# Optimization experiments

Measured on AMD Instinct MI355X. Metric: run time of the kernel, lower is better.

The kernel has to match this reference:

```python
import jax, jax.numpy as jnp
import numpy as np
from jax import lax

INT8_NARROW = (-127.0, 127.0)   # brevitas Int8WeightPerTensorFloat (narrow range)
INT8_FULL = (-128.0, 127.0)     # brevitas Int8ActPerTensorFloat
INT32 = (-2.0**31, 2.0**31 - 1)


def _fake_quant(v, scale, qmin, qmax):
    # round-to-nearest, clip, dequant (per-tensor)
    return jnp.clip(jnp.round(v / scale), qmin, qmax) * scale


def _conv(x, w, stride):
    return lax.conv_general_dilated(
        x, w, window_strides=(stride, stride), padding=[(1, 1), (1, 1)],
        dimension_numbers=("NCHW", "OIHW", "NCHW"))


def setup_inputs() -> dict:
    key = jax.random.key(0)
    ks = jax.random.split(key, 5)
    B, Cin, Cout, H = 64, 256, 512, 28
    x = jax.random.normal(ks[0], (B, Cin, H, H), dtype=jnp.float32)
    w1 = jax.random.normal(ks[1], (Cout, Cin, 3, 3), dtype=jnp.float32) * 0.05
    b1 = jax.random.normal(ks[2], (Cout,), dtype=jnp.float32) * 0.01
    w2 = jax.random.normal(ks[3], (Cout, Cout, 3, 3), dtype=jnp.float32) * 0.05
    b2 = jax.random.normal(ks[4], (Cout,), dtype=jnp.float32) * 0.01
    return {
        "x": x, "w1": w1, "b1": b1, "w2": w2, "b2": b2,
        "in_scale": jnp.full((1,), 0.05, dtype=jnp.float32),
        "act1_scale": jnp.full((1,), 0.05, dtype=jnp.float32),
        "act2_scale": jnp.full((1,), 0.05, dtype=jnp.float32),
    }


def reference(x, w1, b1, w2, b2, in_scale, act1_scale, act2_scale):
    s_in = in_scale[0]
    s_a1 = act1_scale[0]
    s_a2 = act2_scale[0]

    # conv1: per-tensor int8 weight fake-quant (max-abs stats, narrow range)
    s_w1 = jnp.max(jnp.abs(w1)) / 127.0
    wq1 = _fake_quant(w1, s_w1, *INT8_NARROW)
    bq1 = _fake_quant(b1, s_in * s_w1, *INT32)  # Int32Bias: scale = in_scale*w_scale
    out = _conv(x, wq1, 2) + bq1[None, :, None, None]

    # act1: int8 activation fake-quant (learned per-tensor scale)
    out = _fake_quant(out, s_a1, *INT8_FULL)

    # conv2
    s_w2 = jnp.max(jnp.abs(w2)) / 127.0
    wq2 = _fake_quant(w2, s_w2, *INT8_NARROW)
    bq2 = _fake_quant(b2, s_a1 * s_w2, *INT32)
    out = _conv(out, wq2, 1) + bq2[None, :, None, None]

    # act2
    out = _fake_quant(out, s_a2, *INT8_FULL)
    return out
```

## Files before the change

### kernel.cpp

```cpp
#include <hip/hip_runtime.h>

typedef int i32x4 __attribute__((ext_vector_type(4)));

__device__ __forceinline__ void gl_lds16(const signed char* g, signed char* l) {
    __builtin_amdgcn_global_load_lds(
        (const __attribute__((address_space(1))) void*)g,
        (__attribute__((address_space(3))) void*)l, 16, 0, 0);
}

#define XQ_SCALE 2048.0f
#define XQ_DELTA (1.0f / 2048.0f)

__global__ void init_ws_kernel(unsigned* p) {
    if (threadIdx.x < 2) p[threadIdx.x] = 0u;
}

__global__ void absmax2_kernel(const float* __restrict__ w1, const float* __restrict__ w2,
                               unsigned* __restrict__ out) {
    const bool second = blockIdx.x >= 256;
    const float* w = second ? w2 : w1;
    const int n4 = second ? (512 * 512 * 9 / 4) : (512 * 256 * 9 / 4);
    unsigned* o = out + (second ? 1 : 0);
    float m = 0.0f;
    for (int i = (blockIdx.x & 255) * 256 + threadIdx.x; i < n4; i += 65536) {
        float4 v = ((const float4*)w)[i];
        m = fmaxf(m, fmaxf(fmaxf(fabsf(v.x), fabsf(v.y)), fmaxf(fabsf(v.z), fabsf(v.w))));
    }
#pragma unroll
    for (int off = 32; off > 0; off >>= 1)
        m = fmaxf(m, __shfl_down(m, off));
    if ((threadIdx.x & 63) == 0)
        atomicMax(o, __float_as_uint(m));
}

__global__ __launch_bounds__(256) void prep_all_kernel(
    const float* __restrict__ x,
    const float* __restrict__ w1, const float* __restrict__ w2,
    const float* __restrict__ b1, const float* __restrict__ b2,
    const unsigned* __restrict__ absbits,
    const float* __restrict__ in_scale, const float* __restrict__ act1_scale,
    signed char* __restrict__ wq1, signed char* __restrict__ wq2,
    float* __restrict__ bq1, float* __restrict__ bq2,
    signed char* __restrict__ xhi, signed char* __restrict__ xlo,
    signed char* __restrict__ act) {
    __shared__ float t[128][33];
    const int blk = blockIdx.x;
    const int tid = threadIdx.x;
    const uint4 z = {0, 0, 0, 0};

    if (blk < 288) {
        const int thr = blk * 256 + tid;
        const int n = thr / 144;
        const int chunk = thr - n * 144;
        const int r = chunk >> 4;
        const int cin0 = (chunk & 15) * 16;
        const int kh = r / 3;
        const int kw = r - kh * 3;
        const float inv_s = 127.0f / __uint_as_float(absbits[0]);
        union { signed char c[16]; uint4 u; } pk;
#pragma unroll
        for (int j = 0; j < 16; ++j) {
            const float v = w1[((n * 256 + cin0 + j) * 3 + kh) * 3 + kw];
            float q = rintf(v * inv_s);
            q = fminf(fmaxf(q, -127.0f), 127.0f);
            pk.c[j] = (signed char)(int)q;
        }
        *(uint4*)&wq1[n * 2304 + r * 256 + cin0] = pk.u;
    } else if (blk < 864) {
        const int thr = (blk - 288) * 256 + tid;
        const int n = thr / 288;
        const int chunk = thr - n * 288;
        const int r = chunk >> 5;
        const int cin0 = (chunk & 31) * 16;
        const int kh = r / 3;
        const int kw = r - kh * 3;
        const float inv_s = 127.0f / __uint_as_float(absbits[1]);
        union { signed char c[16]; uint4 u; } pk;
#pragma unroll
        for (int j = 0; j < 16; ++j) {
            const float v = w2[((n * 512 + cin0 + j) * 3 + kh) * 3 + kw];
            float q = rintf(v * inv_s);
            q = fminf(fmaxf(q, -127.0f), 127.0f);
            pk.c[j] = (signed char)(int)q;
        }
        *(uint4*)&wq2[n * 4608 + r * 512 + cin0] = pk.u;
    } else if (blk < 868) {
        const int idx = (blk - 864) * 256 + tid;
        if (idx < 512) {
            const float s = (*in_scale) * (__uint_as_float(absbits[0]) * (1.0f / 127.0f));
            float q = rintf(b1[idx] / s);
            q = fminf(fmaxf(q, -2147483648.0f), 2147483648.0f);
            bq1[idx] = q * s;
        } else {
            const int j = idx - 512;
            const float s = (*act1_scale) * (__uint_as_float(absbits[1]) * (1.0f / 127.0f));
            float q = rintf(b2[j] / s);
            q = fminf(fmaxf(q, -2147483648.0f), 2147483648.0f);
            bq2[j] = q * s;
        }
    } else if (blk < 1332) {
        const int thr = (blk - 868) * 256 + tid;
        const int b = thr / (116 * 16);
        const int rr = thr - b * (116 * 16);
        const int p = rr >> 4;
        const int ch = rr & 15;
        int h, w;
        if (p < 30)      { h = 0;          w = p; }
        else if (p < 60) { h = 29;         w = p - 30; }
        else if (p < 88) { h = p - 60 + 1; w = 0; }
        else             { h = p - 88 + 1; w = 29; }
        const int off = (b * 900 + h * 30 + w) * 256 + ch * 16;
        *(uint4*)(xhi + off) = z;
        *(uint4*)(xlo + off) = z;
    } else if (blk < 1812) {
        const int thr = (blk - 1332) * 256 + tid;
        const int b = thr / (60 * 32);
        const int rr = thr - b * (60 * 32);
        const int p = rr >> 5;
        const int ch = rr & 31;
        int h, w;
        if (p < 16)      { h = 0;          w = p; }
        else if (p < 32) { h = 15;         w = p - 16; }
        else if (p < 46) { h = p - 32 + 1; w = 0; }
        else             { h = p - 46 + 1; w = 15; }
        const int off = (b * 256 + h * 16 + w) * 512 + ch * 16;
        *(uint4*)(act + off) = z;
    } else {
        const int xb = blk - 1812;
        const int hwb = xb % 25;
        const int rest = xb / 25;
        const int cb = rest & 1;
        const int b = rest >> 1;
        const int c0 = cb * 128;
        const int hw0 = hwb * 32;
#pragma unroll
        for (int ci = 0; ci < 16; ++ci) {
            const int crow = (tid >> 5) + ci * 8;
            const int hw = hw0 + (tid & 31);
            float v = 0.0f;
            if (hw < 784) v = x[(b * 256 + c0 + crow) * 784 + hw];
            t[crow][tid & 31] = v;
        }
        __syncthreads();
        const int hw_l = tid >> 3;
        const int cg = (tid & 7) * 16;
        const int hw = hw0 + hw_l;
        if (hw < 784) {
            union { signed char c[16]; uint4 u; } ph, pl;
#pragma unroll
            for (int j = 0; j < 16; ++j) {
                const float v = t[cg + j][hw_l];
                int q = (int)rintf(v * XQ_SCALE);
                q = max(-16383, min(16383, q));
                ph.c[j] = (signed char)(q >> 7);
                pl.c[j] = (signed char)(q & 127);
            }
            const int r = hw / 28;
            const int o = (b * 900 + (r + 1) * 30 + (hw - r * 28) + 1) * 256 + c0 + cg;
            *(uint4*)&xhi[o] = ph.u;
            *(uint4*)&xlo[o] = pl.u;
        }
    }
}

template<int CIN, int STRIDE, int HP, int HOUT, bool SPLIT, bool FINAL>
__global__ __launch_bounds__(256, 3) void conv_gemm_kernel(
    const signed char* __restrict__ Ahi,
    const signed char* __restrict__ Alo,
    const signed char* __restrict__ Wt,
    const float* __restrict__ bias,
    const unsigned* __restrict__ wabs,
    const float* __restrict__ s_pre,
    const float* __restrict__ s_act,
    signed char* __restrict__ act_out,
    float* __restrict__ out_final)
{
    constexpr int K = 9 * CIN;
    constexpr int HW = HOUT * HOUT;
    constexpr int LOG2CIN = (CIN == 256) ? 8 : 9;
    constexpr int NC = SPLIT ? 8 : 6;
    constexpr int NACC = SPLIT ? 4 : 2;

    __shared__ __align__(16) signed char As[64 * 128];
    __shared__ __align__(16) signed char As2[SPLIT ? 64 * 128 : 16];
    __shared__ __align__(16) signed char Bs[128 * 128];

    const int tid = threadIdx.x;
    const int lane = tid & 63;
    const int wv = tid >> 6;
    const int wm = wv & 1;
    const int wn = wv >> 1;
    const int quad = lane >> 4;
    const int l16 = lane & 15;
    const int m0 = blockIdx.y * 64;
    const int n0 = blockIdx.x * 128;

    const int lrow = lane >> 3;
    const int koff = ((lane & 7) ^ lrow) * 16;

    const signed char* srcb[NC];
    signed char* dstp[NC];
    bool isA[NC];
#pragma unroll
    for (int i = 0; i < NC; ++i) {
        const int g = wv * NC + i;
        int atype;
        int c;
        if (SPLIT) {
            atype = (g < 8) ? 0 : (g < 16 ? 1 : 2);
            c = (g < 8) ? g : (g < 16 ? g - 8 : g - 16);
        } else {
            atype = (g < 8) ? 0 : 2;
            c = (g < 8) ? g : g - 8;
        }
        if (atype == 2) {
            srcb[i] = Wt + (n0 + c * 8 + lrow) * K + koff;
            dstp[i] = &Bs[c * 1024];
            isA[i] = false;
        } else {
            const int m = m0 + c * 8 + lrow;
            const int b = m / HW;
            const int rem = m - b * HW;
            const int oh = rem / HOUT;
            const int ow = rem - oh * HOUT;
            const int off = ((b * HP + oh * STRIDE) * HP + ow * STRIDE) * CIN + koff;
            srcb[i] = (atype == 0 ? Ahi : Alo) + off;
            dstp[i] = (atype == 0 ? &As[c * 1024] : &As2[c * 1024]);
            isA[i] = true;
        }
    }

    i32x4 acc[NACC][4];
#pragma unroll
    for (int mi = 0; mi < NACC; ++mi)
#pragma unroll
        for (int ni = 0; ni < 4; ++ni)
            acc[mi][ni] = i32x4{0, 0, 0, 0};

    for (int k0 = 0; k0 < K; k0 += 128) {
        const int r9 = k0 >> LOG2CIN;
        const int c0k = k0 & (CIN - 1);
        const int kh = r9 / 3;
        const int kw = r9 - kh * 3;
        const int ashift = (kh * HP + kw) * CIN + c0k;

        __syncthreads();
#pragma unroll
        for (int i = 0; i < NC; ++i)
            gl_lds16(srcb[i] + (isA[i] ? ashift : k0), dstp[i]);
        __syncthreads();

#pragma unroll
        for (int ks = 0; ks < 2; ++ks) {
            i32x4 af[NACC];
            i32x4 bfr[4];
#pragma unroll
            for (int mi = 0; mi < 2; ++mi) {
                const int row = wm * 32 + mi * 16 + l16;
                const int sl = ((ks * 4 + quad) ^ (row & 7)) * 16;
                af[mi] = *(const i32x4*)&As[row * 128 + sl];
                if constexpr (SPLIT)
                    af[mi + 2] = *(const i32x4*)&As2[row * 128 + sl];
            }
#pragma unroll
            for (int ni = 0; ni < 4; ++ni) {
                const int row = wn * 64 + ni * 16 + l16;
                const int sl = ((ks * 4 + quad) ^ (row & 7)) * 16;
                bfr[ni] = *(const i32x4*)&Bs[row * 128 + sl];
            }
#pragma unroll
            for (int mi = 0; mi < 2; ++mi)
#pragma unroll
                for (int ni = 0; ni < 4; ++ni) {
                    acc[mi][ni] = __builtin_amdgcn_mfma_i32_16x16x64_i8(af[mi], bfr[ni], acc[mi][ni], 0, 0, 0);
                    if constexpr (SPLIT)
                        acc[mi + 2][ni] = __builtin_amdgcn_mfma_i32_16x16x64_i8(af[mi + 2], bfr[ni], acc[mi + 2][ni], 0, 0, 0);
                }
        }
    }

    float alpha = __uint_as_float(*wabs) * (1.0f / 127.0f);
    if (FINAL) alpha *= *s_pre;
    if (SPLIT) alpha *= XQ_DELTA;
    const float sact = *s_act;

    float bv[4];
#pragma unroll
    for (int ni = 0; ni < 4; ++ni)
        bv[ni] = bias[n0 + wn * 64 + ni * 16 + l16];

#pragma unroll
    for (int mi = 0; mi < 2; ++mi) {
#pragma unroll
        for (int i = 0; i < 4; ++i) {
            const int m = m0 + wm * 32 + mi * 16 + quad * 4 + i;
            const int b = m / HW;
            const int rem = m - b * HW;
            const int oh = rem / HOUT;
            const int ow = rem - oh * HOUT;
#pragma unroll
            for (int ni = 0; ni < 4; ++ni) {
                const int col = n0 + wn * 64 + ni * 16 + l16;
                int tot = acc[mi][ni][i];
                if constexpr (SPLIT) tot = tot * 128 + acc[mi + 2][ni][i];
                const float v = (float)tot * alpha + bv[ni];
                float q = rintf(v / sact);
                q = fminf(fmaxf(q, -128.0f), 127.0f);
                if (FINAL) {
                    out_final[(b * 512 + col) * HW + oh * HOUT + ow] = q * sact;
                } else {
                    act_out[(b * 256 + (oh + 1) * 16 + (ow + 1)) * 512 + col] = (signed char)(int)q;
                }
            }
        }
    }
}

extern "C" void kernel_launch(void* const* d_in, const int* in_sizes, int n_in,
                              void* d_out, int out_size, void* d_ws, size_t ws_size,
                              hipStream_t stream) {
    const float* x  = (const float*)d_in[0];
    const float* w1 = (const float*)d_in[1];
    const float* b1 = (const float*)d_in[2];
    const float* w2 = (const float*)d_in[3];
    const float* b2 = (const float*)d_in[4];
    const float* in_scale   = (const float*)d_in[5];
    const float* act1_scale = (const float*)d_in[6];
    const float* act2_scale = (const float*)d_in[7];
    float* out = (float*)d_out;

    char* ws = (char*)d_ws;
    unsigned* absbits = (unsigned*)(ws + 0);
    float* bq1 = (float*)(ws + 64);
    float* bq2 = (float*)(ws + 2112);
    signed char* wq1 = (signed char*)(ws + 8192);
    signed char* wq2 = (signed char*)(ws + 1187840);
    signed char* xhi = (signed char*)(ws + 3547136);
    signed char* xlo = (signed char*)(ws + 18292736);
    signed char* act = (signed char*)(ws + 33038336);

    init_ws_kernel<<<1, 64, 0, stream>>>(absbits);
    absmax2_kernel<<<512, 256, 0, stream>>>(w1, w2, absbits);

    prep_all_kernel<<<5012, 256, 0, stream>>>(
        x, w1, w2, b1, b2, absbits, in_scale, act1_scale,
        wq1, wq2, bq1, bq2, xhi, xlo, act);

    conv_gemm_kernel<256, 2, 30, 14, true, false><<<dim3(4, 196), 256, 0, stream>>>(
        xhi, xlo, wq1, bq1, absbits, act1_scale, act1_scale, act, nullptr);

    conv_gemm_kernel<512, 1, 16, 14, false, true><<<dim3(4, 196), 256, 0, stream>>>(
        act, nullptr, wq2, bq2, absbits + 1, act1_scale, act2_scale, nullptr, out);
}
```

Baseline: 265.6 us.

## Double-buffer conv GEMM with 128x128 tiles and coalesce weight quantization

The conv GEMM moves from 64x128 tiles with a 128-wide K step to 128x128 tiles with a 64-wide K step. LDS is now double-buffered, so the global-to-LDS load for the next K slice is issued before the MFMAs on the current one, and a new XOR swizzle suits the 64-byte rows. The weight prep now reads each output channel's weights contiguously and transposes them through shared memory, replacing the strided gathers. The trade-off is a larger register footprint (up to 32 accumulators with the split path), the occupancy hint is dropped, and grid size halves to 392 blocks.

```diff
diff --git a/kernel.cpp b/kernel.cpp
--- a/kernel.cpp
+++ b/kernel.cpp
@@ -43,63 +43,60 @@
     float* __restrict__ bq1, float* __restrict__ bq2,
     signed char* __restrict__ xhi, signed char* __restrict__ xlo,
     signed char* __restrict__ act) {
+    __shared__ __align__(16) signed char sw[4608];
     __shared__ float t[128][33];
     const int blk = blockIdx.x;
     const int tid = threadIdx.x;
     const uint4 z = {0, 0, 0, 0};
 
-    if (blk < 288) {
-        const int thr = blk * 256 + tid;
-        const int n = thr / 144;
-        const int chunk = thr - n * 144;
-        const int r = chunk >> 4;
-        const int cin0 = (chunk & 15) * 16;
-        const int kh = r / 3;
-        const int kw = r - kh * 3;
+    if (blk < 512) {
+        const int n = blk;
         const float inv_s = 127.0f / __uint_as_float(absbits[0]);
-        union { signed char c[16]; uint4 u; } pk;
-#pragma unroll
-        for (int j = 0; j < 16; ++j) {
-            const float v = w1[((n * 256 + cin0 + j) * 3 + kh) * 3 + kw];
+#pragma unroll
+        for (int rd = 0; rd < 9; ++rd) {
+            const int idx = rd * 256 + tid;
+            const float v = w1[n * 2304 + idx];
             float q = rintf(v * inv_s);
             q = fminf(fmaxf(q, -127.0f), 127.0f);
-            pk.c[j] = (signed char)(int)q;
-        }
-        *(uint4*)&wq1[n * 2304 + r * 256 + cin0] = pk.u;
-    } else if (blk < 864) {
-        const int thr = (blk - 288) * 256 + tid;
-        const int n = thr / 288;
-        const int chunk = thr - n * 288;
-        const int r = chunk >> 5;
-        const int cin0 = (chunk & 31) * 16;
-        const int kh = r / 3;
-        const int kw = r - kh * 3;
+            const int cin = idx / 9;
+            const int r = idx - cin * 9;
+            sw[r * 256 + cin] = (signed char)(int)q;
+        }
+        __syncthreads();
+        if (tid < 144) *(uint4*)&wq1[n * 2304 + tid * 16] = *(const uint4*)&sw[tid * 16];
+    } else if (blk < 1024) {
+        const int n = blk - 512;
         const float inv_s = 127.0f / __uint_as_float(absbits[1]);
-        union { signed char c[16]; uint4 u; } pk;
-#pragma unroll
-        for (int j = 0; j < 16; ++j) {
-            const float v = w2[((n * 512 + cin0 + j) * 3 + kh) * 3 + kw];
+#pragma unroll
+        for (int rd = 0; rd < 18; ++rd) {
+            const int idx = rd * 256 + tid;
+            const float v = w2[n * 4608 + idx];
             float q = rintf(v * inv_s);
             q = fminf(fmaxf(q, -127.0f), 127.0f);
-            pk.c[j] = (signed char)(int)q;
-        }
-        *(uint4*)&wq2[n * 4608 + r * 512 + cin0] = pk.u;
-    } else if (blk < 868) {
-        const int idx = (blk - 864) * 256 + tid;
-        if (idx < 512) {
-            const float s = (*in_scale) * (__uint_as_float(absbits[0]) * (1.0f / 127.0f));
-            float q = rintf(b1[idx] / s);
-            q = fminf(fmaxf(q, -2147483648.0f), 2147483648.0f);
-            bq1[idx] = q * s;
-        } else {
-            const int j = idx - 512;
-            const float s = (*act1_scale) * (__uint_as_float(absbits[1]) * (1.0f / 127.0f));
-            float q = rintf(b2[j] / s);
-            q = fminf(fmaxf(q, -2147483648.0f), 2147483648.0f);
-            bq2[j] = q * s;
-        }
-    } else if (blk < 1332) {
-        const int thr = (blk - 868) * 256 + tid;
+            const int cin = idx / 9;
+            const int r = idx - cin * 9;
+            sw[r * 512 + cin] = (signed char)(int)q;
+        }
+        __syncthreads();
+        for (int o = tid; o < 288; o += 256)
+            *(uint4*)&wq2[n * 4608 + o * 16] = *(const uint4*)&sw[o * 16];
+    } else if (blk == 1024) {
+        for (int idx = tid; idx < 1024; idx += 256) {
+            if (idx < 512) {
+                const float s = (*in_scale) * (__uint_as_float(absbits[0]) * (1.0f / 127.0f));
+                float q = rintf(b1[idx] / s);
+                q = fminf(fmaxf(q, -2147483648.0f), 2147483648.0f);
+                bq1[idx] = q * s;
+            } else {
+                const int j = idx - 512;
+                const float s = (*act1_scale) * (__uint_as_float(absbits[1]) * (1.0f / 127.0f));
+                float q = rintf(b2[j] / s);
+                q = fminf(fmaxf(q, -2147483648.0f), 2147483648.0f);
+                bq2[j] = q * s;
+            }
+        }
+    } else if (blk < 1489) {
+        const int thr = (blk - 1025) * 256 + tid;
         const int b = thr / (116 * 16);
         const int rr = thr - b * (116 * 16);
         const int p = rr >> 4;
@@ -112,8 +109,8 @@
         const int off = (b * 900 + h * 30 + w) * 256 + ch * 16;
         *(uint4*)(xhi + off) = z;
         *(uint4*)(xlo + off) = z;
-    } else if (blk < 1812) {
-        const int thr = (blk - 1332) * 256 + tid;
+    } else if (blk < 1969) {
+        const int thr = (blk - 1489) * 256 + tid;
         const int b = thr / (60 * 32);
         const int rr = thr - b * (60 * 32);
         const int p = rr >> 5;
@@ -126,7 +123,7 @@
         const int off = (b * 256 + h * 16 + w) * 512 + ch * 16;
         *(uint4*)(act + off) = z;
     } else {
-        const int xb = blk - 1812;
+        const int xb = blk - 1969;
         const int hwb = xb % 25;
         const int rest = xb / 25;
         const int cb = rest & 1;
@@ -164,7 +161,7 @@
 }
 
 template<int CIN, int STRIDE, int HP, int HOUT, bool SPLIT, bool FINAL>
-__global__ __launch_bounds__(256, 3) void conv_gemm_kernel(
+__global__ __launch_bounds__(256) void conv_gemm_kernel(
     const signed char* __restrict__ Ahi,
     const signed char* __restrict__ Alo,
     const signed char* __restrict__ Wt,
@@ -177,13 +174,13 @@
 {
     constexpr int K = 9 * CIN;
     constexpr int HW = HOUT * HOUT;
-    constexpr int LOG2CIN = (CIN == 256) ? 8 : 9;
-    constexpr int NC = SPLIT ? 8 : 6;
-    constexpr int NACC = SPLIT ? 4 : 2;
-
-    __shared__ __align__(16) signed char As[64 * 128];
-    __shared__ __align__(16) signed char As2[SPLIT ? 64 * 128 : 16];
-    __shared__ __align__(16) signed char Bs[128 * 128];
+    constexpr int NIT = K / 64;
+    constexpr int NC = SPLIT ? 6 : 4;
+    constexpr int NACC = SPLIT ? 8 : 4;
+    constexpr int BUFSZ = SPLIT ? 24576 : 16384;
+    constexpr int BSOFF = SPLIT ? 16384 : 8192;
+
+    __shared__ __align__(16) signed char smem[2][BUFSZ];
 
     const int tid = threadIdx.x;
     const int lane = tid & 63;
@@ -192,40 +189,41 @@
     const int wn = wv >> 1;
     const int quad = lane >> 4;
     const int l16 = lane & 15;
-    const int m0 = blockIdx.y * 64;
+    const int m0 = blockIdx.y * 128;
     const int n0 = blockIdx.x * 128;
 
-    const int lrow = lane >> 3;
-    const int koff = ((lane & 7) ^ lrow) * 16;
+    const int lrow = lane >> 2;
+    const int lslot = lane & 3;
 
     const signed char* srcb[NC];
-    signed char* dstp[NC];
+    int dsto[NC];
     bool isA[NC];
 #pragma unroll
     for (int i = 0; i < NC; ++i) {
         const int g = wv * NC + i;
-        int atype;
-        int c;
+        int type, c;
         if (SPLIT) {
-            atype = (g < 8) ? 0 : (g < 16 ? 1 : 2);
+            type = (g < 8) ? 0 : (g < 16 ? 1 : 2);
             c = (g < 8) ? g : (g < 16 ? g - 8 : g - 16);
         } else {
-            atype = (g < 8) ? 0 : 2;
+            type = (g < 8) ? 0 : 2;
             c = (g < 8) ? g : g - 8;
         }
-        if (atype == 2) {
-            srcb[i] = Wt + (n0 + c * 8 + lrow) * K + koff;
-            dstp[i] = &Bs[c * 1024];
+        const int r = c * 16 + lrow;
+        const int koff = (lslot ^ ((r >> 1) & 3)) * 16;
+        if (type == 2) {
+            srcb[i] = Wt + (n0 + r) * K + koff;
+            dsto[i] = BSOFF + c * 1024;
             isA[i] = false;
         } else {
-            const int m = m0 + c * 8 + lrow;
+            const int m = m0 + r;
             const int b = m / HW;
             const int rem = m - b * HW;
             const int oh = rem / HOUT;
             const int ow = rem - oh * HOUT;
             const int off = ((b * HP + oh * STRIDE) * HP + ow * STRIDE) * CIN + koff;
-            srcb[i] = (atype == 0 ? Ahi : Alo) + off;
-            dstp[i] = (atype == 0 ? &As[c * 1024] : &As2[c * 1024]);
+            srcb[i] = (type == 0 ? Ahi : Alo) + off;
+            dsto[i] = (type == 0 ? 0 : 8192) + c * 1024;
             isA[i] = true;
         }
     }
@@ -237,46 +235,53 @@
         for (int ni = 0; ni < 4; ++ni)
             acc[mi][ni] = i32x4{0, 0, 0, 0};
 
-    for (int k0 = 0; k0 < K; k0 += 128) {
-        const int r9 = k0 >> LOG2CIN;
-        const int c0k = k0 & (CIN - 1);
-        const int kh = r9 / 3;
-        const int kw = r9 - kh * 3;
-        const int ashift = (kh * HP + kw) * CIN + c0k;
-
+    {
+        constexpr int ashift0 = 0;
+#pragma unroll
+        for (int i = 0; i < NC; ++i)
+            gl_lds16(srcb[i] + (isA[i] ? ashift0 : 0), &smem[0][dsto[i]]);
+    }
+
+    int p = 0;
+    for (int it = 0; it < NIT; ++it) {
         __syncthreads();
-#pragma unroll
-        for (int i = 0; i < NC; ++i)
-            gl_lds16(srcb[i] + (isA[i] ? ashift : k0), dstp[i]);
-        __syncthreads();
-
-#pragma unroll
-        for (int ks = 0; ks < 2; ++ks) {
-            i32x4 af[NACC];
-            i32x4 bfr[4];
-#pragma unroll
-            for (int mi = 0; mi < 2; ++mi) {
-                const int row = wm * 32 + mi * 16 + l16;
-                const int sl = ((ks * 4 + quad) ^ (row & 7)) * 16;
-                af[mi] = *(const i32x4*)&As[row * 128 + sl];
+        if (it + 1 < NIT) {
+            const int k0 = (it + 1) * 64;
+            const int r9 = k0 / CIN;
+            const int kh = r9 / 3;
+            const int kw = r9 - kh * 3;
+            const int ashift = (kh * HP + kw) * CIN + (k0 & (CIN - 1));
+            const int q2 = p ^ 1;
+#pragma unroll
+            for (int i = 0; i < NC; ++i)
+                gl_lds16(srcb[i] + (isA[i] ? ashift : k0), &smem[q2][dsto[i]]);
+        }
+
+        i32x4 af[NACC];
+        i32x4 bfr[4];
+#pragma unroll
+        for (int mi = 0; mi < 4; ++mi) {
+            const int row = wm * 64 + mi * 16 + l16;
+            const int sl = (quad ^ ((row >> 1) & 3)) * 16;
+            af[mi] = *(const i32x4*)&smem[p][row * 64 + sl];
+            if constexpr (SPLIT)
+                af[mi + 4] = *(const i32x4*)&smem[p][8192 + row * 64 + sl];
+        }
+#pragma unroll
+        for (int ni = 0; ni < 4; ++ni) {
+            const int row = wn * 64 + ni * 16 + l16;
+            const int sl = (quad ^ ((row >> 1) & 3)) * 16;
+            bfr[ni] = *(const i32x4*)&smem[p][BSOFF + row * 64 + sl];
+        }
+#pragma unroll
+        for (int mi = 0; mi < 4; ++mi)
+#pragma unroll
+            for (int ni = 0; ni < 4; ++ni) {
+                acc[mi][ni] = __builtin_amdgcn_mfma_i32_16x16x64_i8(af[mi], bfr[ni], acc[mi][ni], 0, 0, 0);
                 if constexpr (SPLIT)
-                    af[mi + 2] = *(const i32x4*)&As2[row * 128 + sl];
+                    acc[mi + 4][ni] = __builtin_amdgcn_mfma_i32_16x16x64_i8(af[mi + 4], bfr[ni], acc[mi + 4][ni], 0, 0, 0);
             }
-#pragma unroll
-            for (int ni = 0; ni < 4; ++ni) {
-                const int row = wn * 64 + ni * 16 + l16;
-                const int sl = ((ks * 4 + quad) ^ (row & 7)) * 16;
-                bfr[ni] = *(const i32x4*)&Bs[row * 128 + sl];
-            }
-#pragma unroll
-            for (int mi = 0; mi < 2; ++mi)
-#pragma unroll
-                for (int ni = 0; ni < 4; ++ni) {
-                    acc[mi][ni] = __builtin_amdgcn_mfma_i32_16x16x64_i8(af[mi], bfr[ni], acc[mi][ni], 0, 0, 0);
-                    if constexpr (SPLIT)
-                        acc[mi + 2][ni] = __builtin_amdgcn_mfma_i32_16x16x64_i8(af[mi + 2], bfr[ni], acc[mi + 2][ni], 0, 0, 0);
-                }
-        }
+        p ^= 1;
     }
 
     float alpha = __uint_as_float(*wabs) * (1.0f / 127.0f);
@@ -290,10 +295,10 @@
         bv[ni] = bias[n0 + wn * 64 + ni * 16 + l16];
 
 #pragma unroll
-    for (int mi = 0; mi < 2; ++mi) {
+    for (int mi = 0; mi < 4; ++mi) {
 #pragma unroll
         for (int i = 0; i < 4; ++i) {
-            const int m = m0 + wm * 32 + mi * 16 + quad * 4 + i;
+            const int m = m0 + wm * 64 + mi * 16 + quad * 4 + i;
             const int b = m / HW;
             const int rem = m - b * HW;
             const int oh = rem / HOUT;
@@ -302,7 +307,7 @@
             for (int ni = 0; ni < 4; ++ni) {
                 const int col = n0 + wn * 64 + ni * 16 + l16;
                 int tot = acc[mi][ni][i];
-                if constexpr (SPLIT) tot = tot * 128 + acc[mi + 2][ni][i];
+                if constexpr (SPLIT) tot = tot * 128 + acc[mi + 4][ni][i];
                 const float v = (float)tot * alpha + bv[ni];
                 float q = rintf(v / sact);
                 q = fminf(fmaxf(q, -128.0f), 127.0f);
@@ -342,13 +347,13 @@
     init_ws_kernel<<<1, 64, 0, stream>>>(absbits);
     absmax2_kernel<<<512, 256, 0, stream>>>(w1, w2, absbits);
 
-    prep_all_kernel<<<5012, 256, 0, stream>>>(
+    prep_all_kernel<<<5169, 256, 0, stream>>>(
         x, w1, w2, b1, b2, absbits, in_scale, act1_scale,
         wq1, wq2, bq1, bq2, xhi, xlo, act);
 
-    conv_gemm_kernel<256, 2, 30, 14, true, false><<<dim3(4, 196), 256, 0, stream>>>(
+    conv_gemm_kernel<256, 2, 30, 14, true, false><<<dim3(4, 98), 256, 0, stream>>>(
         xhi, xlo, wq1, bq1, absbits, act1_scale, act1_scale, act, nullptr);
 
-    conv_gemm_kernel<512, 1, 16, 14, false, true><<<dim3(4, 196), 256, 0, stream>>>(
+    conv_gemm_kernel<512, 1, 16, 14, false, true><<<dim3(4, 98), 256, 0, stream>>>(
         act, nullptr, wq2, bq2, absbits + 1, act1_scale, act2_scale, nullptr, out);
 }
```

Measured after the change: 263.7 us. About the same (-0.7%).
